# Kernel tuning notes

Hardware: AMD Instinct MI355X
Metric: run time of the kernel (lower is better)

## Reference

```python
import jax, jax.numpy as jnp
import numpy as np

N_NODES = 100000
N_EDGES = 200000
N_FEAT = 300
HIDDEN = 300
NUM_GRAPHS = 2048
NUM_BOND_TYPE = 6
NUM_BOND_DIR = 3


def setup_inputs() -> dict:
    key = jax.random.key(0)
    ks = jax.random.split(key, 12)
    x = jax.random.normal(ks[0], (N_NODES, N_FEAT), dtype=jnp.float32)
    edge_index = jax.random.randint(ks[1], (2, N_EDGES), 0, N_NODES, dtype=jnp.int64)
    edge_attr = jax.random.randint(ks[2], (N_EDGES, 2), 0, NUM_BOND_DIR, dtype=jnp.int64)
    batch = jnp.sort(jax.random.randint(ks[3], (N_NODES,), 0, NUM_GRAPHS, dtype=jnp.int64))
    s = 1.0 / np.sqrt(N_FEAT)
    emb1 = jax.random.normal(ks[4], (NUM_BOND_TYPE, N_FEAT), dtype=jnp.float32) * s
    emb2 = jax.random.normal(ks[5], (NUM_BOND_DIR, N_FEAT), dtype=jnp.float32) * s
    W1 = jax.random.normal(ks[6], (N_FEAT, 2 * N_FEAT), dtype=jnp.float32) * s
    b1 = jnp.zeros((2 * N_FEAT,), dtype=jnp.float32)
    W2 = jax.random.normal(ks[7], (2 * N_FEAT, HIDDEN), dtype=jnp.float32) * (1.0 / np.sqrt(2 * N_FEAT))
    b2 = jnp.zeros((HIDDEN,), dtype=jnp.float32)
    Wfc = jax.random.normal(ks[8], (HIDDEN, HIDDEN), dtype=jnp.float32) * (1.0 / np.sqrt(HIDDEN))
    bfc = jnp.zeros((HIDDEN,), dtype=jnp.float32)
    return {"x": x, "edge_index": edge_index, "edge_attr": edge_attr, "batch": batch,
            "emb1": emb1, "emb2": emb2, "W1": W1, "b1": b1, "W2": W2, "b2": b2,
            "Wfc": Wfc, "bfc": bfc}


def reference(x, edge_index, edge_attr, batch, emb1, emb2, W1, b1, W2, b2, Wfc, bfc):
    n = x.shape[0]
    # add_self_loops(fill_value=0): append N self edges with zero edge_attr
    loop = jnp.arange(n, dtype=edge_index.dtype)
    src = jnp.concatenate([edge_index[0], loop])  # [E+N]
    dst = jnp.concatenate([edge_index[1], loop])
    ea = jnp.concatenate([edge_attr, jnp.zeros((n, 2), dtype=edge_attr.dtype)], axis=0)
    # edge embeddings (shared by both conv layers)
    edge_emb = emb1[ea[:, 0]] + emb2[ea[:, 1]]  # [E+N, F]

    def mlp(h):
        return jax.nn.relu(h @ W1 + b1) @ W2 + b2

    def gin(h):
        # message: x_j + edge_emb, scatter-add at target nodes, then shared MLP
        msg = h[src] + edge_emb
        aggr = jax.ops.segment_sum(msg, dst, num_segments=n)
        return mlp(aggr)

    h = jax.nn.relu(gin(x))
    h = jax.nn.relu(gin(h))
    # global_add_pool over graphs in batch
    g = jax.ops.segment_sum(h, batch, num_segments=NUM_GRAPHS)  # [G, H]
    return g @ Wfc + bfc
```

## Files before the change

kernel.cpp:

```cpp
#include <hip/hip_runtime.h>
#include <hip/hip_bf16.h>

#define NFEAT 300
#define KP 320
#define NGRAPH 2048
#define N1P 640
#define N2P 384
#define NTD 18
#define SCAN_B 2048

typedef __bf16 bf16x8 __attribute__((ext_vector_type(8)));
typedef float  f32x4  __attribute__((ext_vector_type(4)));
typedef unsigned short u16x8 __attribute__((ext_vector_type(8)));

__device__ __forceinline__ unsigned short f2b(float v) {
    union { float f; unsigned u; } x; x.f = v;
    unsigned r = x.u + 0x7fff + ((x.u >> 16) & 1);
    return (unsigned short)(r >> 16);
}
__device__ __forceinline__ float b2f(unsigned short u) {
    union { unsigned u; float f; } x; x.u = ((unsigned)u) << 16;
    return x.f;
}

#define GLD_LDS16(g, l)                                                        \
    __builtin_amdgcn_global_load_lds(                                          \
        (const __attribute__((address_space(1))) void*)(g),                    \
        (__attribute__((address_space(3))) void*)(l), 16, 0, 0)

__global__ __launch_bounds__(256) void k_embc(
    const float* __restrict__ emb1, const float* __restrict__ emb2,
    float* __restrict__ embc)
{
    int t = blockIdx.x * blockDim.x + threadIdx.x;
    if (t >= NTD * KP) return;
    int td = t / KP, c = t % KP;
    int t1 = td / 3, d = td % 3;
    embc[t] = (c < NFEAT) ? emb1[t1 * NFEAT + c] + emb2[d * NFEAT + c] : 0.f;
}

__global__ __launch_bounds__(256) void k_zero(int* __restrict__ p, int n)
{
    int i = blockIdx.x * blockDim.x + threadIdx.x;
    if (i < n) p[i] = 0;
}

__global__ __launch_bounds__(256) void k_deg(
    const int* __restrict__ ei, int* __restrict__ deg, int E)
{
    int e = blockIdx.x * blockDim.x + threadIdx.x;
    if (e >= E) return;
    atomicAdd(&deg[ei[E + e]], 1);
}

__global__ __launch_bounds__(256) void k_scan1(
    const int* __restrict__ deg, int* __restrict__ offsets,
    int* __restrict__ bsum, int n)
{
    __shared__ int sh[256];
    int tid = threadIdx.x;
    int base = blockIdx.x * SCAN_B + tid * 8;
    int v[8], run = 0;
#pragma unroll
    for (int j = 0; j < 8; ++j) {
        int i = base + j;
        v[j] = (i < n) ? deg[i] : 0;
        run += v[j];
        v[j] = run;
    }
    sh[tid] = run;
    __syncthreads();
    for (int off = 1; off < 256; off <<= 1) {
        int t = (tid >= off) ? sh[tid - off] : 0;
        __syncthreads();
        sh[tid] += t;
        __syncthreads();
    }
    int excl = sh[tid] - run;
#pragma unroll
    for (int j = 0; j < 8; ++j) {
        int i = base + j;
        if (i < n) offsets[i + 1] = excl + v[j];
    }
    if (tid == 0) bsum[blockIdx.x] = sh[255];
}

__global__ void k_scan2(int* __restrict__ bsum, int nb, int* __restrict__ offsets)
{
    if (threadIdx.x == 0 && blockIdx.x == 0) {
        int run = 0;
        for (int b = 0; b < nb; ++b) { int t = bsum[b]; bsum[b] = run; run += t; }
        offsets[0] = 0;
    }
}

__global__ __launch_bounds__(256) void k_scan3(
    const int* __restrict__ deg, int* __restrict__ offsets,
    const int* __restrict__ bsum, int* __restrict__ cursor, int n)
{
    int i = blockIdx.x * blockDim.x + threadIdx.x;
    if (i >= n) return;
    int fin = offsets[i + 1] + bsum[i / SCAN_B];
    offsets[i + 1] = fin;
    cursor[i] = fin - deg[i];
}

__global__ __launch_bounds__(256) void k_fill(
    const int* __restrict__ ei, const int* __restrict__ ea,
    int* __restrict__ cursor, int* __restrict__ edgerec, int E)
{
    int e = blockIdx.x * blockDim.x + threadIdx.x;
    if (e >= E) return;
    int dst = ei[E + e];
    int pos = atomicAdd(&cursor[dst], 1);
    int src = ei[e];
    int td  = ea[2 * e] * 3 + ea[2 * e + 1];
    edgerec[pos] = src | (td << 20);
}

__global__ __launch_bounds__(256) void k_aggr_b16(
    const unsigned short* __restrict__ h,
    const int* __restrict__ offsets, const int* __restrict__ edgerec,
    const float* __restrict__ embc,
    unsigned short* __restrict__ Ab, int n, int Mpad)
{
    int idx = blockIdx.x * blockDim.x + threadIdx.x;
    if (idx >= Mpad * (KP / 8)) return;
    int v = idx / (KP / 8), c0 = (idx % (KP / 8)) * 8;
    unsigned short* outp = &Ab[(size_t)v * KP + c0];
    if (v >= n) {
        *(uint4*)outp = make_uint4(0, 0, 0, 0);
        return;
    }
    float acc[8];
    u16x8 hv = *(const u16x8*)&h[(size_t)v * KP + c0];
    const float* e0 = embc + c0;
#pragma unroll
    for (int j = 0; j < 8; ++j) acc[j] = b2f(hv[j]) + e0[j];

    int beg = offsets[v], end = offsets[v + 1];
    for (int e = beg; e < end; ++e) {
        int rec = edgerec[e];
        int src = rec & 0xFFFFF;
        int td  = rec >> 20;
        u16x8 hs = *(const u16x8*)&h[(size_t)src * KP + c0];
        const float* ee = embc + td * KP + c0;
#pragma unroll
        for (int j = 0; j < 8; ++j) acc[j] += b2f(hs[j]) + ee[j];
    }
    unsigned short o[8];
#pragma unroll
    for (int j = 0; j < 8; ++j) o[j] = f2b(acc[j]);
    *(uint4*)outp = *(uint4*)o;
}

__global__ __launch_bounds__(256) void k_aggr_f32(
    const float* __restrict__ x,
    const int* __restrict__ offsets, const int* __restrict__ edgerec,
    const float* __restrict__ embc,
    unsigned short* __restrict__ Ab, int n, int Mpad)
{
    int idx = blockIdx.x * blockDim.x + threadIdx.x;
    if (idx >= Mpad * (KP / 8)) return;
    int v = idx / (KP / 8), c0 = (idx % (KP / 8)) * 8;
    unsigned short* outp = &Ab[(size_t)v * KP + c0];
    if (v >= n || c0 >= 304) {
        if (v < Mpad) *(uint4*)outp = make_uint4(0, 0, 0, 0);
        return;
    }
    bool full = (c0 + 8 <= NFEAT);

    float acc[8];
    {
        const float* row = x + (size_t)v * NFEAT + c0;
        if (full) {
            float4 a = *(const float4*)row, b = *(const float4*)(row + 4);
            acc[0] = a.x; acc[1] = a.y; acc[2] = a.z; acc[3] = a.w;
            acc[4] = b.x; acc[5] = b.y; acc[6] = b.z; acc[7] = b.w;
        } else {
#pragma unroll
            for (int j = 0; j < 8; ++j)
                acc[j] = (c0 + j < NFEAT) ? row[j] : 0.f;
        }
        const float* e0 = embc + c0;
#pragma unroll
        for (int j = 0; j < 8; ++j) acc[j] += e0[j];
    }

    int beg = offsets[v], end = offsets[v + 1];
    for (int e = beg; e < end; ++e) {
        int rec = edgerec[e];
        int src = rec & 0xFFFFF;
        int td  = rec >> 20;
        const float* row = x + (size_t)src * NFEAT + c0;
        const float* ee  = embc + td * KP + c0;
        if (full) {
            float4 a = *(const float4*)row, b = *(const float4*)(row + 4);
            acc[0] += a.x + ee[0]; acc[1] += a.y + ee[1];
            acc[2] += a.z + ee[2]; acc[3] += a.w + ee[3];
            acc[4] += b.x + ee[4]; acc[5] += b.y + ee[5];
            acc[6] += b.z + ee[6]; acc[7] += b.w + ee[7];
        } else {
#pragma unroll
            for (int j = 0; j < 8; ++j)
                acc[j] += ((c0 + j < NFEAT) ? row[j] : 0.f) + ee[j];
        }
    }
    unsigned short o[8];
#pragma unroll
    for (int j = 0; j < 8; ++j) o[j] = f2b(acc[j]);
    *(uint4*)outp = *(uint4*)o;
}

__global__ __launch_bounds__(256) void k_cvtW(
    const float* __restrict__ W, unsigned short* __restrict__ Wt,
    int rows, int cols, int Kpad, int Npad)
{
    int t = blockIdx.x * blockDim.x + threadIdx.x;
    if (t >= Npad * Kpad) return;
    int nn = t / Kpad, k = t % Kpad;
    float v = (k < rows && nn < cols) ? W[(size_t)k * cols + nn] : 0.f;
    Wt[t] = f2b(v);
}

__global__ __launch_bounds__(256) void k_gemm(
    const unsigned short* __restrict__ Ag, const unsigned short* __restrict__ Bg,
    const float* __restrict__ bias, int bias_n,
    unsigned short* __restrict__ C, int ldc, int store_cols,
    int K, int npass, int MT)
{
    __shared__ unsigned short smem[16384];

    int tid  = threadIdx.x;
    int lane = tid & 63, wave = tid >> 6;

    int l    = blockIdx.x;
    int xcd  = l & 7;
    int j    = l >> 3;
    int ncol = j % npass;
    int panel= (j / npass) * 8 + xcd;
    if (panel >= MT) return;
    int m0 = panel * 128;

    int wm = (wave >> 1) * 64, wn = (wave & 1) * 64;
    int fr = lane & 15, fq = lane >> 4;
    int colq = lane & 15, rq = (lane >> 4) * 4;

    const unsigned short* Abase = Ag + (size_t)m0 * K;
    const unsigned short* Bbase = Bg + (size_t)ncol * 128 * K;

    int c0 = tid, c1 = 256 + tid;
    size_t aoff0 = (size_t)(c0 >> 2) * K + 8 * ((c0 & 3) ^ ((c0 >> 3) & 3));
    size_t aoff1 = (size_t)(c1 >> 2) * K + 8 * ((c1 & 3) ^ ((c1 >> 3) & 3));

    int fswz = 8 * (fq ^ ((fr >> 1) & 3));

    f32x4 acc[4][4];
#pragma unroll
    for (int i = 0; i < 4; ++i)
#pragma unroll
        for (int jj = 0; jj < 4; ++jj)
            acc[i][jj] = (f32x4){0.f, 0.f, 0.f, 0.f};

    int niter = K >> 5;

    GLD_LDS16(Abase + aoff0, &smem[c0 * 8]);
    GLD_LDS16(Abase + aoff1, &smem[c1 * 8]);
    GLD_LDS16(Bbase + aoff0, &smem[4096 + c0 * 8]);
    GLD_LDS16(Bbase + aoff1, &smem[4096 + c1 * 8]);
    __syncthreads();

    for (int i = 0; i < niter; ++i) {
        int cur = (i & 1) << 13;
        int nxt = 8192 - cur;
        if (i + 1 < niter) {
            int k0 = (i + 1) * 32;
            GLD_LDS16(Abase + aoff0 + k0, &smem[nxt + c0 * 8]);
            GLD_LDS16(Abase + aoff1 + k0, &smem[nxt + c1 * 8]);
            GLD_LDS16(Bbase + aoff0 + k0, &smem[nxt + 4096 + c0 * 8]);
            GLD_LDS16(Bbase + aoff1 + k0, &smem[nxt + 4096 + c1 * 8]);
        }

        bf16x8 af[4], bfv[4];
#pragma unroll
        for (int i2 = 0; i2 < 4; ++i2) {
            af[i2]  = *(const bf16x8*)&smem[cur + (wm + i2 * 16 + fr) * 32 + fswz];
            bfv[i2] = *(const bf16x8*)&smem[cur + 4096 + (wn + i2 * 16 + fr) * 32 + fswz];
        }
#pragma unroll
        for (int i2 = 0; i2 < 4; ++i2)
#pragma unroll
            for (int jj = 0; jj < 4; ++jj)
                acc[i2][jj] = __builtin_amdgcn_mfma_f32_16x16x32_bf16(
                    af[i2], bfv[jj], acc[i2][jj], 0, 0, 0);
        __syncthreads();
    }

#pragma unroll
    for (int ch = 0; ch < 2; ++ch) {
        if ((wn >> 6) == ch) {
#pragma unroll
            for (int jj = 0; jj < 4; ++jj) {
                int lc  = jj * 16 + colq;
                int col = ncol * 128 + wn + jj * 16 + colq;
                float bv = (col < bias_n) ? bias[col] : 0.f;
#pragma unroll
                for (int i = 0; i < 4; ++i) {
                    int rbase = wm + i * 16 + rq;
#pragma unroll
                    for (int r = 0; r < 4; ++r) {
                        float v = fmaxf(acc[i][jj][r] + bv, 0.f);
                        smem[(rbase + r) * 64 + lc] = f2b(v);
                    }
                }
            }
        }
        __syncthreads();
        int cbase = ncol * 128 + ch * 64;
        if (cbase < store_cols) {
#pragma unroll
            for (int i = 0; i < 4; ++i) {
                int idx = i * 256 + tid;
                int row = idx >> 3, c8 = idx & 7;
                *(uint4*)&C[(size_t)(m0 + row) * ldc + cbase + c8 * 8] =
                    *(uint4*)&smem[row * 64 + c8 * 8];
            }
        }
        __syncthreads();
    }
}

__global__ __launch_bounds__(64) void k_pool(
    const unsigned short* __restrict__ H, const int* __restrict__ batch,
    float* __restrict__ g, int n)
{
    int gid = blockIdx.x;
    int lo = 0, hi = n;
    while (lo < hi) { int mid = (lo + hi) >> 1; if (batch[mid] < gid) lo = mid + 1; else hi = mid; }
    int start = lo;
    hi = n;
    while (lo < hi) { int mid = (lo + hi) >> 1; if (batch[mid] < gid + 1) lo = mid + 1; else hi = mid; }
    int end = lo;

    int ch = threadIdx.x;
    if (ch >= KP / 8) return;
    int c0 = ch * 8;
    float acc[8];
#pragma unroll
    for (int j = 0; j < 8; ++j) acc[j] = 0.f;
    for (int v = start; v < end; ++v) {
        u16x8 hv = *(const u16x8*)&H[(size_t)v * KP + c0];
#pragma unroll
        for (int j = 0; j < 8; ++j) acc[j] += b2f(hv[j]);
    }
#pragma unroll
    for (int j = 0; j < 8; ++j)
        if (c0 + j < NFEAT) g[(size_t)gid * NFEAT + c0 + j] = acc[j];
}

__global__ __launch_bounds__(256) void k_final(
    const float* __restrict__ g, const float* __restrict__ Wfc,
    const float* __restrict__ bfc, float* __restrict__ out)
{
    int idx = blockIdx.x * blockDim.x + threadIdx.x;
    if (idx >= NGRAPH * NFEAT) return;
    int r = idx / NFEAT, c = idx % NFEAT;
    float acc = bfc[c];
    for (int k = 0; k < NFEAT; ++k)
        acc = fmaf(g[(size_t)r * NFEAT + k], Wfc[(size_t)k * NFEAT + c], acc);
    out[idx] = acc;
}

extern "C" void kernel_launch(void* const* d_in, const int* in_sizes, int n_in,
                              void* d_out, int out_size, void* d_ws, size_t ws_size,
                              hipStream_t stream)
{
    const float* x    = (const float*)d_in[0];
    const int*   ei   = (const int*)  d_in[1];
    const int*   ea   = (const int*)  d_in[2];
    const int*   batch= (const int*)  d_in[3];
    const float* emb1 = (const float*)d_in[4];
    const float* emb2 = (const float*)d_in[5];
    const float* W1   = (const float*)d_in[6];
    const float* b1   = (const float*)d_in[7];
    const float* W2   = (const float*)d_in[8];
    const float* b2   = (const float*)d_in[9];
    const float* Wfc  = (const float*)d_in[10];
    const float* bfc  = (const float*)d_in[11];
    float* out = (float*)d_out;

    int n = in_sizes[0] / NFEAT;
    int E = in_sizes[1] / 2;
    int MT   = (n + 127) / 128;
    int Mpad = MT * 128;
    int MT8  = ((MT + 7) / 8) * 8;

    char* p = (char*)d_ws;
    auto take = [&](size_t bytes) { char* r = p; p += (bytes + 255) & ~(size_t)255; return r; };
    unsigned short* T    = (unsigned short*)take((size_t)Mpad * N1P * 2);
    unsigned short* Ab   = (unsigned short*)take((size_t)Mpad * KP * 2);
    unsigned short* Hb   = (unsigned short*)take((size_t)Mpad * KP * 2);
    unsigned short* Wt1  = (unsigned short*)take((size_t)N1P * KP * 2);
    unsigned short* Wt2  = (unsigned short*)take((size_t)N2P * N1P * 2);
    float*          embc = (float*)take((size_t)NTD * KP * 4);
    float*          g    = (float*)take((size_t)NGRAPH * NFEAT * 4);
    int*            deg  = (int*)take((size_t)n * 4);
    int*            offs = (int*)take((size_t)(n + 1) * 4);
    int*            curs = (int*)take((size_t)n * 4);
    int*            erec = (int*)take((size_t)E * 4);
    int*            bsum = (int*)take(256 * 4);

    dim3 blk(256);
    int chunkThreads = Mpad * (KP / 8);
    int chunkBlocks  = (chunkThreads + 255) / 256;
    int nb = (n + SCAN_B - 1) / SCAN_B;

    k_cvtW<<<(N1P * KP + 255) / 256, blk, 0, stream>>>(W1, Wt1, NFEAT, 600, KP, N1P);
    k_cvtW<<<(N2P * N1P + 255) / 256, blk, 0, stream>>>(W2, Wt2, 600, NFEAT, N1P, N2P);
    k_embc<<<(NTD * KP + 255) / 256, blk, 0, stream>>>(emb1, emb2, embc);

    k_zero <<<(n + 255) / 256, blk, 0, stream>>>(deg, n);
    k_deg  <<<(E + 255) / 256, blk, 0, stream>>>(ei, deg, E);
    k_scan1<<<nb, blk, 0, stream>>>(deg, offs, bsum, n);
    k_scan2<<<1, 64, 0, stream>>>(bsum, nb, offs);
    k_scan3<<<(n + 255) / 256, blk, 0, stream>>>(deg, offs, bsum, curs, n);
    k_fill <<<(E + 255) / 256, blk, 0, stream>>>(ei, ea, curs, erec, E);

    k_aggr_f32<<<chunkBlocks, blk, 0, stream>>>(x, offs, erec, embc, Ab, n, Mpad);
    k_gemm<<<MT8 * (N1P / 128), blk, 0, stream>>>(Ab, Wt1, b1, 600, T, N1P, N1P, KP, N1P / 128, MT);
    k_gemm<<<MT8 * (N2P / 128), blk, 0, stream>>>(T, Wt2, b2, NFEAT, Hb, KP, KP, N1P, N2P / 128, MT);

    k_aggr_b16<<<chunkBlocks, blk, 0, stream>>>(Hb, offs, erec, embc, Ab, n, Mpad);
    k_gemm<<<MT8 * (N1P / 128), blk, 0, stream>>>(Ab, Wt1, b1, 600, T, N1P, N1P, KP, N1P / 128, MT);
    k_gemm<<<MT8 * (N2P / 128), blk, 0, stream>>>(T, Wt2, b2, NFEAT, Hb, KP, KP, N1P, N2P / 128, MT);

    k_pool <<<NGRAPH, 64, 0, stream>>>(Hb, batch, g, n);
    k_final<<<(NGRAPH * NFEAT + 255) / 256, blk, 0, stream>>>(g, Wfc, bfc, out);
}
```

Before: 750.5 us.

## Widen GEMM tile to 128x256 with half-width fallback for tail columns

The GEMM block now computes a 128x256 output tile (each wave does 64x128), with a runtime fallback to 128x128 when fewer than 256 columns remain. This halves the number of times each A panel is reloaded across column blocks and raises MFMA work per LDS A-fragment load. In exchange, LDS use grows to 48KB, each thread holds twice the accumulator registers, and the grid gets fewer blocks. For N=384 one block of each pair runs the narrow path, which may unbalance the load.

```diff
diff --git a/kernel.cpp b/kernel.cpp
--- a/kernel.cpp
+++ b/kernel.cpp
@@ -223,13 +223,13 @@
     Wt[t] = f2b(v);
 }
 
-__global__ __launch_bounds__(256) void k_gemm(
+__global__ __launch_bounds__(256, 2) void k_gemm(
     const unsigned short* __restrict__ Ag, const unsigned short* __restrict__ Bg,
     const float* __restrict__ bias, int bias_n,
     unsigned short* __restrict__ C, int ldc, int store_cols,
-    int K, int npass, int MT)
-{
-    __shared__ unsigned short smem[16384];
+    int K, int ngrp, int Npad, int MT)
+{
+    __shared__ unsigned short smem[24576];
 
     int tid  = threadIdx.x;
     int lane = tid & 63, wave = tid >> 6;
@@ -237,72 +237,94 @@
     int l    = blockIdx.x;
     int xcd  = l & 7;
     int j    = l >> 3;
-    int ncol = j % npass;
-    int panel= (j / npass) * 8 + xcd;
+    int ncol = j % ngrp;
+    int panel= (j / ngrp) * 8 + xcd;
     if (panel >= MT) return;
     int m0 = panel * 128;
-
-    int wm = (wave >> 1) * 64, wn = (wave & 1) * 64;
+    int n0 = ncol * 256;
+    bool do2 = (n0 + 256 <= Npad);
+    int wcols = do2 ? 128 : 64;
+
+    int wm  = (wave >> 1) * 64;
+    int wn2 = (wave & 1) * wcols;
     int fr = lane & 15, fq = lane >> 4;
     int colq = lane & 15, rq = (lane >> 4) * 4;
 
     const unsigned short* Abase = Ag + (size_t)m0 * K;
-    const unsigned short* Bbase = Bg + (size_t)ncol * 128 * K;
-
-    int c0 = tid, c1 = 256 + tid;
-    size_t aoff0 = (size_t)(c0 >> 2) * K + 8 * ((c0 & 3) ^ ((c0 >> 3) & 3));
-    size_t aoff1 = (size_t)(c1 >> 2) * K + 8 * ((c1 & 3) ^ ((c1 >> 3) & 3));
+    const unsigned short* Bbase = Bg + (size_t)n0 * K;
+
+    int ca0 = tid, ca1 = tid + 256;
+    int cb0 = tid, cb1 = tid + 256;
+    int cb2 = tid + 512, cb3 = tid + 768;
+#define CHOFF(c) ((size_t)((c) >> 2) * K + 8 * (((c) & 3) ^ (((c) >> 3) & 3)))
+    size_t a0 = CHOFF(ca0), a1 = CHOFF(ca1);
+    size_t b0 = CHOFF(cb0), b1 = CHOFF(cb1), b2 = CHOFF(cb2), b3 = CHOFF(cb3);
 
     int fswz = 8 * (fq ^ ((fr >> 1) & 3));
 
-    f32x4 acc[4][4];
+    f32x4 acc[4][8];
 #pragma unroll
     for (int i = 0; i < 4; ++i)
 #pragma unroll
-        for (int jj = 0; jj < 4; ++jj)
+        for (int jj = 0; jj < 8; ++jj)
             acc[i][jj] = (f32x4){0.f, 0.f, 0.f, 0.f};
 
     int niter = K >> 5;
 
-    GLD_LDS16(Abase + aoff0, &smem[c0 * 8]);
-    GLD_LDS16(Abase + aoff1, &smem[c1 * 8]);
-    GLD_LDS16(Bbase + aoff0, &smem[4096 + c0 * 8]);
-    GLD_LDS16(Bbase + aoff1, &smem[4096 + c1 * 8]);
+    GLD_LDS16(Abase + a0, &smem[ca0 * 8]);
+    GLD_LDS16(Abase + a1, &smem[ca1 * 8]);
+    GLD_LDS16(Bbase + b0, &smem[4096 + cb0 * 8]);
+    GLD_LDS16(Bbase + b1, &smem[4096 + cb1 * 8]);
+    if (do2) {
+        GLD_LDS16(Bbase + b2, &smem[4096 + cb2 * 8]);
+        GLD_LDS16(Bbase + b3, &smem[4096 + cb3 * 8]);
+    }
     __syncthreads();
 
     for (int i = 0; i < niter; ++i) {
-        int cur = (i & 1) << 13;
-        int nxt = 8192 - cur;
+        int cur = (i & 1) ? 12288 : 0;
+        int nxt = 12288 - cur;
         if (i + 1 < niter) {
             int k0 = (i + 1) * 32;
-            GLD_LDS16(Abase + aoff0 + k0, &smem[nxt + c0 * 8]);
-            GLD_LDS16(Abase + aoff1 + k0, &smem[nxt + c1 * 8]);
-            GLD_LDS16(Bbase + aoff0 + k0, &smem[nxt + 4096 + c0 * 8]);
-            GLD_LDS16(Bbase + aoff1 + k0, &smem[nxt + 4096 + c1 * 8]);
-        }
-
-        bf16x8 af[4], bfv[4];
-#pragma unroll
-        for (int i2 = 0; i2 < 4; ++i2) {
-            af[i2]  = *(const bf16x8*)&smem[cur + (wm + i2 * 16 + fr) * 32 + fswz];
-            bfv[i2] = *(const bf16x8*)&smem[cur + 4096 + (wn + i2 * 16 + fr) * 32 + fswz];
-        }
+            GLD_LDS16(Abase + a0 + k0, &smem[nxt + ca0 * 8]);
+            GLD_LDS16(Abase + a1 + k0, &smem[nxt + ca1 * 8]);
+            GLD_LDS16(Bbase + b0 + k0, &smem[nxt + 4096 + cb0 * 8]);
+            GLD_LDS16(Bbase + b1 + k0, &smem[nxt + 4096 + cb1 * 8]);
+            if (do2) {
+                GLD_LDS16(Bbase + b2 + k0, &smem[nxt + 4096 + cb2 * 8]);
+                GLD_LDS16(Bbase + b3 + k0, &smem[nxt + 4096 + cb3 * 8]);
+            }
+        }
+
+        bf16x8 af[4];
 #pragma unroll
         for (int i2 = 0; i2 < 4; ++i2)
-#pragma unroll
-            for (int jj = 0; jj < 4; ++jj)
-                acc[i2][jj] = __builtin_amdgcn_mfma_f32_16x16x32_bf16(
-                    af[i2], bfv[jj], acc[i2][jj], 0, 0, 0);
+            af[i2] = *(const bf16x8*)&smem[cur + (wm + i2 * 16 + fr) * 32 + fswz];
+#pragma unroll
+        for (int jj = 0; jj < 8; ++jj) {
+            if (do2 || jj < 4) {
+                bf16x8 bv = *(const bf16x8*)
+                    &smem[cur + 4096 + (wn2 + jj * 16 + fr) * 32 + fswz];
+#pragma unroll
+                for (int i2 = 0; i2 < 4; ++i2)
+                    acc[i2][jj] = __builtin_amdgcn_mfma_f32_16x16x32_bf16(
+                        af[i2], bv, acc[i2][jj], 0, 0, 0);
+            }
+        }
         __syncthreads();
     }
 
-#pragma unroll
-    for (int ch = 0; ch < 2; ++ch) {
-        if ((wn >> 6) == ch) {
-#pragma unroll
-            for (int jj = 0; jj < 4; ++jj) {
-                int lc  = jj * 16 + colq;
-                int col = ncol * 128 + wn + jj * 16 + colq;
+    int nch   = do2 ? 4 : 2;
+    int chlo  = wn2 >> 6;
+    int nown  = do2 ? 2 : 1;
+    for (int ch = 0; ch < nch; ++ch) {
+        if (ch >= chlo && ch < chlo + nown) {
+            int jjb = do2 ? ((ch & 1) * 4) : 0;
+#pragma unroll
+            for (int dj = 0; dj < 4; ++dj) {
+                int jj  = jjb + dj;
+                int lc  = dj * 16 + colq;
+                int col = n0 + ch * 64 + dj * 16 + colq;
                 float bv = (col < bias_n) ? bias[col] : 0.f;
 #pragma unroll
                 for (int i = 0; i < 4; ++i) {
@@ -316,7 +338,7 @@
             }
         }
         __syncthreads();
-        int cbase = ncol * 128 + ch * 64;
+        int cbase = n0 + ch * 64;
         if (cbase < store_cols) {
 #pragma unroll
             for (int i = 0; i < 4; ++i) {
@@ -328,6 +350,7 @@
         }
         __syncthreads();
     }
+#undef CHOFF
 }
 
 __global__ __launch_bounds__(64) void k_pool(
@@ -426,13 +449,16 @@
     k_scan3<<<(n + 255) / 256, blk, 0, stream>>>(deg, offs, bsum, curs, n);
     k_fill <<<(E + 255) / 256, blk, 0, stream>>>(ei, ea, curs, erec, E);
 
+    int ng1 = (N1P + 255) / 256;
+    int ng2 = (N2P + 255) / 256;
+
     k_aggr_f32<<<chunkBlocks, blk, 0, stream>>>(x, offs, erec, embc, Ab, n, Mpad);
-    k_gemm<<<MT8 * (N1P / 128), blk, 0, stream>>>(Ab, Wt1, b1, 600, T, N1P, N1P, KP, N1P / 128, MT);
-    k_gemm<<<MT8 * (N2P / 128), blk, 0, stream>>>(T, Wt2, b2, NFEAT, Hb, KP, KP, N1P, N2P / 128, MT);
+    k_gemm<<<MT8 * ng1, blk, 0, stream>>>(Ab, Wt1, b1, 600, T, N1P, N1P, KP, ng1, N1P, MT);
+    k_gemm<<<MT8 * ng2, blk, 0, stream>>>(T, Wt2, b2, NFEAT, Hb, KP, KP, N1P, ng2, N2P, MT);
 
     k_aggr_b16<<<chunkBlocks, blk, 0, stream>>>(Hb, offs, erec, embc, Ab, n, Mpad);
-    k_gemm<<<MT8 * (N1P / 128), blk, 0, stream>>>(Ab, Wt1, b1, 600, T, N1P, N1P, KP, N1P / 128, MT);
-    k_gemm<<<MT8 * (N2P / 128), blk, 0, stream>>>(T, Wt2, b2, NFEAT, Hb, KP, KP, N1P, N2P / 128, MT);
+    k_gemm<<<MT8 * ng1, blk, 0, stream>>>(Ab, Wt1, b1, 600, T, N1P, N1P, KP, ng1, N1P, MT);
+    k_gemm<<<MT8 * ng2, blk, 0, stream>>>(T, Wt2, b2, NFEAT, Hb, KP, KP, N1P, ng2, N2P, MT);
 
     k_pool <<<NGRAPH, 64, 0, stream>>>(Hb, batch, g, n);
     k_final<<<(NGRAPH * NFEAT + 255) / 256, blk, 0, stream>>>(g, Wfc, bfc, out);
```

New measurement: 2.722 ms. 3.63x slower.
